# Performance work log

Measured on AMD Instinct MI355X. Metric: run time of the kernel, lower is better.

Reference implementation:

```python
import jax, jax.numpy as jnp
import numpy as np


def _cif_cmat(w_seq):
    """Integrate-and-fire assignment matrix for one sequence.
    w_seq: [T] sigmoid weights. Returns [T, T+1] (T+1 is a static upper
    bound on the number of fired output frames)."""
    T = w_seq.shape[0]
    cols = jnp.arange(T + 1)

    def step(carry, w):
        acc, k = carry
        fire = acc + w > 1.0
        on_k = (cols == k).astype(w.dtype)
        on_k1 = (cols == k + 1).astype(w.dtype)
        row_fire = on_k * (1.0 - acc) / w + on_k1 * (acc + w - 1.0) / w
        row = jnp.where(fire, row_fire, on_k)
        acc_new = jnp.where(fire, jnp.zeros_like(acc), acc + w)  # original resets acc to 0
        k_new = jnp.where(fire, k + 1, k)
        return (acc_new, k_new), row

    init = (jnp.zeros((), w_seq.dtype), jnp.zeros((), jnp.int32))
    _, rows = jax.lax.scan(step, init, w_seq)
    return rows  # [T, T+1]


def setup_inputs() -> dict:
    key = jax.random.key(0)
    k1, k2, k3 = jax.random.split(key, 3)
    B, T, D = 8, 2000, 512
    feat = jax.random.normal(k1, (B, T, D), dtype=jnp.float32)
    hlens = jax.random.randint(k2, (B,), 0, T).astype(jnp.int32)
    W = jax.random.normal(k3, (D,), dtype=jnp.float32) * (1.0 / np.sqrt(D))
    b = jnp.zeros((1,), dtype=jnp.float32)
    return {"feat": feat, "hlens": hlens, "W": W, "b": b}


def reference(feat, hlens, W, b):
    # weight = sigmoid(Linear(feat))  -> [B, T]
    weight = jax.nn.sigmoid(jnp.einsum("btd,d->bt", feat, W) + b[0])
    hlens_new = jnp.ceil(jnp.sum(weight, axis=1)).astype(jnp.int32)
    # sequential integrate-and-fire scan, vmapped over batch -> [B, T, T+1]
    weight_cmat = jax.lax.stop_gradient(jax.vmap(_cif_cmat)(weight))
    weight_mat = weight[:, :, None] * weight_cmat        # [B, T, M]
    feat_new = jnp.einsum("btd,btm->bmd", feat, weight_mat)  # [B, M, D]
    return feat_new, hlens_new
```

## Files before the change

### kernel.cpp

```cpp
#include <hip/hip_runtime.h>
#include <math.h>

#define BATCH 8
#define TLEN 2000
#define DIM 512
#define MLEN (TLEN + 1)
#define NTH 1024
#define MAXLVL 11

__global__ __launch_bounds__(256) void weight_kernel(
    const float* __restrict__ feat, const float* __restrict__ W,
    const float* __restrict__ bias, float* __restrict__ weight) {
  int gwave = (blockIdx.x * 256 + threadIdx.x) >> 6;
  int lane  = threadIdx.x & 63;
  if (gwave >= BATCH * TLEN) return;
  const float4* f4 = (const float4*)feat + (size_t)gwave * (DIM / 4) + lane * 2;
  const float4* w4 = (const float4*)W + lane * 2;
  float4 a0 = f4[0], a1 = f4[1];
  float4 b0 = w4[0], b1 = w4[1];
  float s = a0.x * b0.x + a0.y * b0.y + a0.z * b0.z + a0.w * b0.w +
            a1.x * b1.x + a1.y * b1.y + a1.z * b1.z + a1.w * b1.w;
#pragma unroll
  for (int off = 32; off > 0; off >>= 1) s += __shfl_xor(s, off, 64);
  if (lane == 0) {
    float x = s + bias[0];
    weight[gwave] = 1.0f / (1.0f + expf(-x));
  }
}

__global__ __launch_bounds__(NTH) void scan_kernel(
    const float* __restrict__ weight, float* __restrict__ hlens_out,
    int4* __restrict__ AB) {
  int b = blockIdx.x;
  int tid = threadIdx.x;
  int lane = tid & 63, wid = tid >> 6;

  __shared__ float w_s[TLEN];
  __shared__ float S_s[TLEN];
  __shared__ float wtot[16];
  __shared__ unsigned short Ga_s[MLEN];
  __shared__ unsigned short Gb_s[MLEN];
  __shared__ unsigned short F_s[2048];
  __shared__ int done_lv[MAXLVL];
  __shared__ int K_s;

  const float* wrow = weight + b * TLEN;
  int base = tid * 2;
  float w0 = 0.f, w1 = 0.f;
  if (base < TLEN) {
    float2 v = *(const float2*)(wrow + base);
    w0 = v.x; w1 = v.y;
  }
  float mysum = w0 + w1;
  float sc = mysum;
#pragma unroll
  for (int d = 1; d < 64; d <<= 1) {
    float o = __shfl_up(sc, d, 64);
    if (lane >= d) sc += o;
  }
  if (lane == 63) wtot[wid] = sc;
  if (tid < MAXLVL) done_lv[tid] = 1;
  __syncthreads();
  float woff = 0.f;
  for (int j = 0; j < wid; j++) woff += wtot[j];
  float excl = woff + (sc - mysum);
  if (base < TLEN) {
    w_s[base] = w0; w_s[base + 1] = w1;
    S_s[base] = excl + w0;
    S_s[base + 1] = excl + w0 + w1;
  }
  if (tid == 0) {
    float tot = 0.f;
    for (int j = 0; j < 16; j++) tot += wtot[j];
    hlens_out[b] = ceilf(tot);
  }
  __syncthreads();

  {
    int l0 = tid + 1, r0 = TLEN;  float tg0 = S_s[tid] + 1.0f;
    int s1v = tid + 1024;
    bool has1 = (s1v < TLEN);
    int l1 = has1 ? s1v + 1 : TLEN, r1 = TLEN;
    float tg1 = has1 ? S_s[s1v] + 1.0f : 0.f;
    bool has2 = (tid == 0);
    int l2 = 0, r2 = has2 ? TLEN : 0;
#pragma unroll
    for (int step = 0; step < MAXLVL; step++) {
      if (l0 < r0) { int m = (l0 + r0) >> 1; if (S_s[m] > tg0) r0 = m; else l0 = m + 1; }
      if (l1 < r1) { int m = (l1 + r1) >> 1; if (S_s[m] > tg1) r1 = m; else l1 = m + 1; }
      if (l2 < r2) { int m = (l2 + r2) >> 1; if (S_s[m] > 1.0f) r2 = m; else l2 = m + 1; }
    }
    Ga_s[tid] = (unsigned short)l0;
    if (has1) Ga_s[s1v] = (unsigned short)l1;
    F_s[tid] = (unsigned short)TLEN;
    F_s[tid + 1024] = (unsigned short)TLEN;
    if (tid == 0) {
      Ga_s[TLEN] = (unsigned short)TLEN;
      F_s[0] = (unsigned short)l2;
    }
  }
  __syncthreads();

  {
    unsigned short* cur = Ga_s;
    unsigned short* nxt = Gb_s;
    int flen = 1;
    for (int lvl = 0; lvl < MAXLVL; lvl++) {
      int s0 = tid, s1v = tid + 1024;
      int g20 = (int)cur[cur[s0]];
      int g21 = (s1v <= TLEN) ? (int)cur[cur[s1v]] : TLEN;
      int i0 = tid, i1 = tid + 1024;
      int nv0 = -1, nv1 = -1;
      if (i0 < flen) nv0 = (int)cur[F_s[i0]];
      if (i1 < flen) nv1 = (int)cur[F_s[i1]];
      nxt[s0] = (unsigned short)g20;
      if (s1v <= TLEN) nxt[s1v] = (unsigned short)g21;
      if (i0 < flen) { F_s[flen + i0] = (unsigned short)nv0; if (nv0 < TLEN) done_lv[lvl] = 0; }
      if (i1 < flen) { F_s[flen + i1] = (unsigned short)nv1; if (nv1 < TLEN) done_lv[lvl] = 0; }
      __syncthreads();
      flen <<= 1;
      unsigned short* t = cur; cur = nxt; nxt = t;
      if (done_lv[lvl]) break;
    }
  }

#pragma unroll
  for (int it = 0; it < 2; it++) {
    int k = tid + it * 1024;
    if ((int)F_s[k] == TLEN && (k == 0 || (int)F_s[k - 1] < TLEN)) K_s = k;
  }
  __syncthreads();
  int K = K_s;

#pragma unroll
  for (int it = 0; it < 2; it++) {
    int m = tid + it * 1024;
    if (m >= MLEN) continue;
    int a, e;
    float cL = 0.f, cR = 0.f;
    if (m == 0) {
      a = 0;
      if (K > 0) {
        e = (int)F_s[0];
        cR = 1.0f - ((e > 0) ? S_s[e - 1] : 0.f);
      } else {
        e = TLEN - 1;
        cR = w_s[TLEN - 1];
      }
    } else if (m <= K) {
      int f1 = (int)F_s[m - 1];
      float Sp0 = (m >= 2) ? S_s[(int)F_s[m - 2]] : 0.f;
      a = f1;
      cL = S_s[f1] - Sp0 - 1.0f;
      if (m < K) {
        e = (int)F_s[m];
        cR = 1.0f - (S_s[e - 1] - S_s[f1]);
      } else {
        e = TLEN - 1;
        cR = w_s[TLEN - 1];
      }
    } else {
      a = 0x7fffffff; e = -1;
    }
    int4 pk;
    pk.x = a; pk.y = e;
    pk.z = __float_as_int(cL);
    pk.w = __float_as_int(cR);
    AB[(size_t)b * MLEN + m] = pk;
  }
}

__global__ __launch_bounds__(256) void gather_kernel(
    const float* __restrict__ feat, const float* __restrict__ weight,
    const int4* __restrict__ AB, float* __restrict__ out) {
  int bm = (blockIdx.x * 256 + threadIdx.x) >> 6;
  int lane = threadIdx.x & 63;
  if (bm >= BATCH * MLEN) return;
  int b = bm / MLEN, m = bm % MLEN;
  int4 ab = AB[(size_t)bm];
  int a = ab.x, e = ab.y;
  float cL = __int_as_float(ab.z), cR = __int_as_float(ab.w);
  float4 acc0 = {0.f, 0.f, 0.f, 0.f};
  float4 acc1 = {0.f, 0.f, 0.f, 0.f};
  const float4* f4 = (const float4*)feat + (size_t)b * TLEN * (DIM / 4) + lane * 2;
  const float* wrow = weight + b * TLEN;
  for (int t = a; t <= e; t++) {
    float c = (t == a && m > 0) ? cL : ((t == e) ? cR : wrow[t]);
    const float4* fr = f4 + (size_t)t * (DIM / 4);
    float4 fa = fr[0], fb = fr[1];
    acc0.x += c * fa.x; acc0.y += c * fa.y; acc0.z += c * fa.z; acc0.w += c * fa.w;
    acc1.x += c * fb.x; acc1.y += c * fb.y; acc1.z += c * fb.z; acc1.w += c * fb.w;
  }
  float4* orow = (float4*)out + (size_t)bm * (DIM / 4) + lane * 2;
  orow[0] = acc0;
  orow[1] = acc1;
}

extern "C" void kernel_launch(void* const* d_in, const int* in_sizes, int n_in,
                              void* d_out, int out_size, void* d_ws, size_t ws_size,
                              hipStream_t stream) {
  const float* feat = (const float*)d_in[0];
  const float* W    = (const float*)d_in[2];
  const float* bias = (const float*)d_in[3];

  float* out       = (float*)d_out;
  float* feat_new  = out;
  float* hlens_out = out + (size_t)BATCH * MLEN * DIM;

  char* ws = (char*)d_ws;
  float* weight = (float*)ws;
  int4*  AB     = (int4*)(ws + 64000);

  weight_kernel<<<(BATCH * TLEN) / 4, 256, 0, stream>>>(feat, W, bias, weight);
  scan_kernel<<<BATCH, NTH, 0, stream>>>(weight, hlens_out, AB);
  int nframes = BATCH * MLEN;
  gather_kernel<<<(nframes + 3) / 4, 256, 0, stream>>>(feat, weight, AB, feat_new);
}
```

Before: 100.6 us.

## Fuse weight, scan and gather into one cooperative kernel with grid syncs

Merges the three separate launches (weight dot-product, per-batch integrate-and-fire scan, frame gather) into a single cooperative kernel separated by grid-wide syncs. The weight and gather phases become grid-stride loops over a fixed 1024-block grid. The scan phase is reworked for 256 threads, each handling 8 elements. The aim is to remove launch overhead and the inter-kernel gaps. In exchange, the scan runs on only 8 blocks while the rest of the grid waits at the barrier, and the fixed-grid strided gather may balance variable-length frames less evenly.

```diff
diff --git a/kernel.cpp b/kernel.cpp
--- a/kernel.cpp
+++ b/kernel.cpp
@@ -1,199 +1,230 @@
 #include <hip/hip_runtime.h>
+#include <hip/hip_cooperative_groups.h>
 #include <math.h>
+
+namespace cg = cooperative_groups;
 
 #define BATCH 8
 #define TLEN 2000
 #define DIM 512
 #define MLEN (TLEN + 1)
-#define NTH 1024
 #define MAXLVL 11
-
-__global__ __launch_bounds__(256) void weight_kernel(
+#define GRID 1024
+#define BLK 256
+
+__global__ __launch_bounds__(BLK) void fused_kernel(
     const float* __restrict__ feat, const float* __restrict__ W,
-    const float* __restrict__ bias, float* __restrict__ weight) {
-  int gwave = (blockIdx.x * 256 + threadIdx.x) >> 6;
-  int lane  = threadIdx.x & 63;
-  if (gwave >= BATCH * TLEN) return;
-  const float4* f4 = (const float4*)feat + (size_t)gwave * (DIM / 4) + lane * 2;
-  const float4* w4 = (const float4*)W + lane * 2;
-  float4 a0 = f4[0], a1 = f4[1];
-  float4 b0 = w4[0], b1 = w4[1];
-  float s = a0.x * b0.x + a0.y * b0.y + a0.z * b0.z + a0.w * b0.w +
-            a1.x * b1.x + a1.y * b1.y + a1.z * b1.z + a1.w * b1.w;
-#pragma unroll
-  for (int off = 32; off > 0; off >>= 1) s += __shfl_xor(s, off, 64);
-  if (lane == 0) {
-    float x = s + bias[0];
-    weight[gwave] = 1.0f / (1.0f + expf(-x));
-  }
-}
-
-__global__ __launch_bounds__(NTH) void scan_kernel(
-    const float* __restrict__ weight, float* __restrict__ hlens_out,
-    int4* __restrict__ AB) {
-  int b = blockIdx.x;
+    const float* __restrict__ bias, float* __restrict__ weight,
+    float* __restrict__ hlens_out, int4* __restrict__ AB,
+    float* __restrict__ out) {
+  cg::grid_group grid = cg::this_grid();
   int tid = threadIdx.x;
   int lane = tid & 63, wid = tid >> 6;
-
-  __shared__ float w_s[TLEN];
+  int gwave = (int)((blockIdx.x * BLK + tid) >> 6);
+  int nwaves = (int)((gridDim.x * BLK) >> 6);
+
   __shared__ float S_s[TLEN];
-  __shared__ float wtot[16];
   __shared__ unsigned short Ga_s[MLEN];
   __shared__ unsigned short Gb_s[MLEN];
   __shared__ unsigned short F_s[2048];
+  __shared__ float wtot[4];
   __shared__ int done_lv[MAXLVL];
   __shared__ int K_s;
 
-  const float* wrow = weight + b * TLEN;
-  int base = tid * 2;
-  float w0 = 0.f, w1 = 0.f;
-  if (base < TLEN) {
-    float2 v = *(const float2*)(wrow + base);
-    w0 = v.x; w1 = v.y;
+  {
+    const float4* w4 = (const float4*)W + lane * 2;
+    float4 b0 = w4[0], b1 = w4[1];
+    float bb = bias[0];
+    for (int row = gwave; row < BATCH * TLEN; row += nwaves) {
+      const float4* f4 = (const float4*)feat + (size_t)row * (DIM / 4) + lane * 2;
+      float4 a0 = f4[0], a1 = f4[1];
+      float s = a0.x * b0.x + a0.y * b0.y + a0.z * b0.z + a0.w * b0.w +
+                a1.x * b1.x + a1.y * b1.y + a1.z * b1.z + a1.w * b1.w;
+#pragma unroll
+      for (int off = 32; off > 0; off >>= 1) s += __shfl_xor(s, off, 64);
+      if (lane == 0) weight[row] = 1.0f / (1.0f + expf(-(s + bb)));
+    }
   }
-  float mysum = w0 + w1;
-  float sc = mysum;
-#pragma unroll
-  for (int d = 1; d < 64; d <<= 1) {
-    float o = __shfl_up(sc, d, 64);
-    if (lane >= d) sc += o;
+  grid.sync();
+
+  if (blockIdx.x < BATCH) {
+    int b = blockIdx.x;
+    const float* wrow = weight + b * TLEN;
+
+    int base = tid * 8;
+    float loc[8];
+    float mysum = 0.f;
+    bool act = (base + 8 <= TLEN);
+    if (act) {
+      float4 v0 = *(const float4*)(wrow + base);
+      float4 v1 = *(const float4*)(wrow + base + 4);
+      float wv[8] = {v0.x, v0.y, v0.z, v0.w, v1.x, v1.y, v1.z, v1.w};
+      float run = 0.f;
+#pragma unroll
+      for (int j = 0; j < 8; j++) { run += wv[j]; loc[j] = run; }
+      mysum = run;
+    }
+    float sc = mysum;
+#pragma unroll
+    for (int d = 1; d < 64; d <<= 1) {
+      float o = __shfl_up(sc, d, 64);
+      if (lane >= d) sc += o;
+    }
+    if (lane == 63) wtot[wid] = sc;
+    if (tid < MAXLVL) done_lv[tid] = 1;
+    __syncthreads();
+    float woff = 0.f;
+    for (int j = 0; j < wid; j++) woff += wtot[j];
+    float excl = woff + (sc - mysum);
+    if (act) {
+#pragma unroll
+      for (int j = 0; j < 8; j++) S_s[base + j] = excl + loc[j];
+    }
+    if (tid == 0)
+      hlens_out[b] = ceilf(wtot[0] + wtot[1] + wtot[2] + wtot[3]);
+    __syncthreads();
+
+    {
+      int l[8], r[8];
+      float tg[8];
+#pragma unroll
+      for (int it = 0; it < 8; it++) {
+        int s = tid + it * 256;
+        if (s < TLEN - 1) { l[it] = s + 1; r[it] = TLEN; tg[it] = S_s[s] + 1.0f; }
+        else             { l[it] = TLEN;  r[it] = TLEN; tg[it] = 0.f; }
+      }
+#pragma unroll
+      for (int step = 0; step < MAXLVL; step++) {
+#pragma unroll
+        for (int it = 0; it < 8; it++) {
+          if (l[it] < r[it]) {
+            int mid = (l[it] + r[it]) >> 1;
+            if (S_s[mid] > tg[it]) r[it] = mid; else l[it] = mid + 1;
+          }
+        }
+      }
+#pragma unroll
+      for (int it = 0; it < 8; it++) {
+        int s = tid + it * 256;
+        if (s <= TLEN) Ga_s[s] = (unsigned short)l[it];
+        F_s[tid + it * 256] = (unsigned short)TLEN;
+      }
+      if (tid == 0) {
+        Ga_s[TLEN] = (unsigned short)TLEN;
+        int l2 = 0, r2 = TLEN;
+        while (l2 < r2) { int m = (l2 + r2) >> 1; if (S_s[m] > 1.0f) r2 = m; else l2 = m + 1; }
+        F_s[0] = (unsigned short)l2;
+      }
+    }
+    __syncthreads();
+
+    {
+      unsigned short* cur = Ga_s;
+      unsigned short* nxt = Gb_s;
+      int flen = 1;
+      for (int lvl = 0; lvl < MAXLVL; lvl++) {
+        int g2[8], nv[8];
+#pragma unroll
+        for (int it = 0; it < 8; it++) {
+          int s = tid + it * 256;
+          g2[it] = (s <= TLEN) ? (int)cur[cur[s]] : TLEN;
+        }
+#pragma unroll
+        for (int it = 0; it < 8; it++) {
+          int i = tid + it * 256;
+          nv[it] = (i < flen) ? (int)cur[F_s[i]] : -1;
+        }
+#pragma unroll
+        for (int it = 0; it < 8; it++) {
+          int s = tid + it * 256;
+          if (s <= TLEN) nxt[s] = (unsigned short)g2[it];
+        }
+#pragma unroll
+        for (int it = 0; it < 8; it++) {
+          int i = tid + it * 256;
+          if (i < flen) {
+            F_s[flen + i] = (unsigned short)nv[it];
+            if (nv[it] < TLEN) done_lv[lvl] = 0;
+          }
+        }
+        __syncthreads();
+        flen <<= 1;
+        unsigned short* t = cur; cur = nxt; nxt = t;
+        if (done_lv[lvl]) break;
+      }
+    }
+
+#pragma unroll
+    for (int it = 0; it < 8; it++) {
+      int k = tid + it * 256;
+      if ((int)F_s[k] == TLEN && (k == 0 || (int)F_s[k - 1] < TLEN)) K_s = k;
+    }
+    __syncthreads();
+    int K = K_s;
+    float wlast = wrow[TLEN - 1];
+
+#pragma unroll
+    for (int it = 0; it < 8; it++) {
+      int m = tid + it * 256;
+      if (m >= MLEN) continue;
+      int a, e;
+      float cL = 0.f, cR = 0.f;
+      if (m == 0) {
+        a = 0;
+        if (K > 0) {
+          e = (int)F_s[0];
+          cR = 1.0f - ((e > 0) ? S_s[e - 1] : 0.f);
+        } else {
+          e = TLEN - 1;
+          cR = wlast;
+        }
+      } else if (m <= K) {
+        int f1 = (int)F_s[m - 1];
+        float Sp0 = (m >= 2) ? S_s[(int)F_s[m - 2]] : 0.f;
+        a = f1;
+        cL = S_s[f1] - Sp0 - 1.0f;
+        if (m < K) {
+          e = (int)F_s[m];
+          cR = 1.0f - (S_s[e - 1] - S_s[f1]);
+        } else {
+          e = TLEN - 1;
+          cR = wlast;
+        }
+      } else {
+        a = 0x7fffffff; e = -1;
+      }
+      int4 pk;
+      pk.x = a; pk.y = e;
+      pk.z = __float_as_int(cL);
+      pk.w = __float_as_int(cR);
+      AB[(size_t)b * MLEN + m] = pk;
+    }
   }
-  if (lane == 63) wtot[wid] = sc;
-  if (tid < MAXLVL) done_lv[tid] = 1;
-  __syncthreads();
-  float woff = 0.f;
-  for (int j = 0; j < wid; j++) woff += wtot[j];
-  float excl = woff + (sc - mysum);
-  if (base < TLEN) {
-    w_s[base] = w0; w_s[base + 1] = w1;
-    S_s[base] = excl + w0;
-    S_s[base + 1] = excl + w0 + w1;
+  grid.sync();
+
+  {
+    const int nfr = BATCH * MLEN;
+    for (int bm = gwave; bm < nfr; bm += nwaves) {
+      int b = bm / MLEN, m = bm % MLEN;
+      int4 ab = AB[(size_t)bm];
+      int a = ab.x, e = ab.y;
+      float cL = __int_as_float(ab.z), cR = __int_as_float(ab.w);
+      float4 acc0 = {0.f, 0.f, 0.f, 0.f};
+      float4 acc1 = {0.f, 0.f, 0.f, 0.f};
+      const float4* f4 = (const float4*)feat + (size_t)b * TLEN * (DIM / 4) + lane * 2;
+      const float* wrow = weight + b * TLEN;
+      for (int t = a; t <= e; t++) {
+        float c = (t == a && m > 0) ? cL : ((t == e) ? cR : wrow[t]);
+        const float4* fr = f4 + (size_t)t * (DIM / 4);
+        float4 fa = fr[0], fb = fr[1];
+        acc0.x += c * fa.x; acc0.y += c * fa.y; acc0.z += c * fa.z; acc0.w += c * fa.w;
+        acc1.x += c * fb.x; acc1.y += c * fb.y; acc1.z += c * fb.z; acc1.w += c * fb.w;
+      }
+      float4* orow = (float4*)out + (size_t)bm * (DIM / 4) + lane * 2;
+      orow[0] = acc0;
+      orow[1] = acc1;
+    }
   }
-  if (tid == 0) {
-    float tot = 0.f;
-    for (int j = 0; j < 16; j++) tot += wtot[j];
-    hlens_out[b] = ceilf(tot);
-  }
-  __syncthreads();
-
-  {
-    int l0 = tid + 1, r0 = TLEN;  float tg0 = S_s[tid] + 1.0f;
-    int s1v = tid + 1024;
-    bool has1 = (s1v < TLEN);
-    int l1 = has1 ? s1v + 1 : TLEN, r1 = TLEN;
-    float tg1 = has1 ? S_s[s1v] + 1.0f : 0.f;
-    bool has2 = (tid == 0);
-    int l2 = 0, r2 = has2 ? TLEN : 0;
-#pragma unroll
-    for (int step = 0; step < MAXLVL; step++) {
-      if (l0 < r0) { int m = (l0 + r0) >> 1; if (S_s[m] > tg0) r0 = m; else l0 = m + 1; }
-      if (l1 < r1) { int m = (l1 + r1) >> 1; if (S_s[m] > tg1) r1 = m; else l1 = m + 1; }
-      if (l2 < r2) { int m = (l2 + r2) >> 1; if (S_s[m] > 1.0f) r2 = m; else l2 = m + 1; }
-    }
-    Ga_s[tid] = (unsigned short)l0;
-    if (has1) Ga_s[s1v] = (unsigned short)l1;
-    F_s[tid] = (unsigned short)TLEN;
-    F_s[tid + 1024] = (unsigned short)TLEN;
-    if (tid == 0) {
-      Ga_s[TLEN] = (unsigned short)TLEN;
-      F_s[0] = (unsigned short)l2;
-    }
-  }
-  __syncthreads();
-
-  {
-    unsigned short* cur = Ga_s;
-    unsigned short* nxt = Gb_s;
-    int flen = 1;
-    for (int lvl = 0; lvl < MAXLVL; lvl++) {
-      int s0 = tid, s1v = tid + 1024;
-      int g20 = (int)cur[cur[s0]];
-      int g21 = (s1v <= TLEN) ? (int)cur[cur[s1v]] : TLEN;
-      int i0 = tid, i1 = tid + 1024;
-      int nv0 = -1, nv1 = -1;
-      if (i0 < flen) nv0 = (int)cur[F_s[i0]];
-      if (i1 < flen) nv1 = (int)cur[F_s[i1]];
-      nxt[s0] = (unsigned short)g20;
-      if (s1v <= TLEN) nxt[s1v] = (unsigned short)g21;
-      if (i0 < flen) { F_s[flen + i0] = (unsigned short)nv0; if (nv0 < TLEN) done_lv[lvl] = 0; }
-      if (i1 < flen) { F_s[flen + i1] = (unsigned short)nv1; if (nv1 < TLEN) done_lv[lvl] = 0; }
-      __syncthreads();
-      flen <<= 1;
-      unsigned short* t = cur; cur = nxt; nxt = t;
-      if (done_lv[lvl]) break;
-    }
-  }
-
-#pragma unroll
-  for (int it = 0; it < 2; it++) {
-    int k = tid + it * 1024;
-    if ((int)F_s[k] == TLEN && (k == 0 || (int)F_s[k - 1] < TLEN)) K_s = k;
-  }
-  __syncthreads();
-  int K = K_s;
-
-#pragma unroll
-  for (int it = 0; it < 2; it++) {
-    int m = tid + it * 1024;
-    if (m >= MLEN) continue;
-    int a, e;
-    float cL = 0.f, cR = 0.f;
-    if (m == 0) {
-      a = 0;
-      if (K > 0) {
-        e = (int)F_s[0];
-        cR = 1.0f - ((e > 0) ? S_s[e - 1] : 0.f);
-      } else {
-        e = TLEN - 1;
-        cR = w_s[TLEN - 1];
-      }
-    } else if (m <= K) {
-      int f1 = (int)F_s[m - 1];
-      float Sp0 = (m >= 2) ? S_s[(int)F_s[m - 2]] : 0.f;
-      a = f1;
-      cL = S_s[f1] - Sp0 - 1.0f;
-      if (m < K) {
-        e = (int)F_s[m];
-        cR = 1.0f - (S_s[e - 1] - S_s[f1]);
-      } else {
-        e = TLEN - 1;
-        cR = w_s[TLEN - 1];
-      }
-    } else {
-      a = 0x7fffffff; e = -1;
-    }
-    int4 pk;
-    pk.x = a; pk.y = e;
-    pk.z = __float_as_int(cL);
-    pk.w = __float_as_int(cR);
-    AB[(size_t)b * MLEN + m] = pk;
-  }
-}
-
-__global__ __launch_bounds__(256) void gather_kernel(
-    const float* __restrict__ feat, const float* __restrict__ weight,
-    const int4* __restrict__ AB, float* __restrict__ out) {
-  int bm = (blockIdx.x * 256 + threadIdx.x) >> 6;
-  int lane = threadIdx.x & 63;
-  if (bm >= BATCH * MLEN) return;
-  int b = bm / MLEN, m = bm % MLEN;
-  int4 ab = AB[(size_t)bm];
-  int a = ab.x, e = ab.y;
-  float cL = __int_as_float(ab.z), cR = __int_as_float(ab.w);
-  float4 acc0 = {0.f, 0.f, 0.f, 0.f};
-  float4 acc1 = {0.f, 0.f, 0.f, 0.f};
-  const float4* f4 = (const float4*)feat + (size_t)b * TLEN * (DIM / 4) + lane * 2;
-  const float* wrow = weight + b * TLEN;
-  for (int t = a; t <= e; t++) {
-    float c = (t == a && m > 0) ? cL : ((t == e) ? cR : wrow[t]);
-    const float4* fr = f4 + (size_t)t * (DIM / 4);
-    float4 fa = fr[0], fb = fr[1];
-    acc0.x += c * fa.x; acc0.y += c * fa.y; acc0.z += c * fa.z; acc0.w += c * fa.w;
-    acc1.x += c * fb.x; acc1.y += c * fb.y; acc1.z += c * fb.z; acc1.w += c * fb.w;
-  }
-  float4* orow = (float4*)out + (size_t)bm * (DIM / 4) + lane * 2;
-  orow[0] = acc0;
-  orow[1] = acc1;
 }
 
 extern "C" void kernel_launch(void* const* d_in, const int* in_sizes, int n_in,
@@ -204,15 +235,14 @@
   const float* bias = (const float*)d_in[3];
 
   float* out       = (float*)d_out;
-  float* feat_new  = out;
   float* hlens_out = out + (size_t)BATCH * MLEN * DIM;
 
   char* ws = (char*)d_ws;
   float* weight = (float*)ws;
   int4*  AB     = (int4*)(ws + 64000);
 
-  weight_kernel<<<(BATCH * TLEN) / 4, 256, 0, stream>>>(feat, W, bias, weight);
-  scan_kernel<<<BATCH, NTH, 0, stream>>>(weight, hlens_out, AB);
-  int nframes = BATCH * MLEN;
-  gather_kernel<<<(nframes + 3) / 4, 256, 0, stream>>>(feat, weight, AB, feat_new);
+  void* kargs[] = {(void*)&feat, (void*)&W, (void*)&bias, (void*)&weight,
+                   (void*)&hlens_out, (void*)&AB, (void*)&out};
+  hipLaunchCooperativeKernel((const void*)fused_kernel, dim3(GRID), dim3(BLK),
+                             kargs, 0, stream);
 }
```

Result: slower. 274.8 us (+173.3%).
